# Performance work log

Measured on AMD Instinct MI355X. Metric: run time of the kernel, lower is better.

## Reference

```python
import jax, jax.numpy as jnp
import numpy as np

HIDDEN = 2048
FFN = 2048      # ffn_hidden_size (tp_size == 1)
E = 8           # moe_num_experts
TOP_K = 2       # moe_top_k
S = 2048        # number of tokens


def setup_inputs() -> dict:
    key = jax.random.key(0)
    k1, k2, k3, k4 = jax.random.split(key, 4)
    return {
        "hidden_states": jax.random.normal(k1, (S, HIDDEN), jnp.float32),
        "w_qkv": jax.random.normal(k2, (3 * E, HIDDEN), jnp.float32) * 0.02,
        "w1": jax.random.normal(k3, (E, HIDDEN, 2 * FFN), jnp.float32) * 0.02,
        "w2": jax.random.normal(k4, (E, FFN, HIDDEN), jnp.float32) * 0.02,
        "top_k": TOP_K,
    }


def reference(hidden_states, w_qkv, w1, w2, top_k):
    S, H = hidden_states.shape
    # --- ParallelAttention_router (gate), computed in fp32 as in the source ---
    mix = hidden_states @ w_qkv.T                                  # [S, 3E]
    q, k, v = jnp.split(mix.astype(jnp.float32), 3, axis=-1)       # each [S, E]
    # attn_weights[s,i,j] = q[s,i]*k[s,j]; softmax over j; logits = attn @ v
    attn = jax.nn.softmax(q[:, :, None] * k[:, None, :], axis=-1)  # [S, E, E]
    logits = jnp.einsum('sij,sj->si', attn, v)                     # [S, E]
    # --- top-k routing: softmax over selected logits ---
    top_logits, indices = jax.lax.top_k(logits, top_k)             # [S, K]
    scores = jax.nn.softmax(top_logits, axis=-1).astype(hidden_states.dtype)
    # --- experts: per-expert GLU MLP. The torch code sorts tokens by expert and
    # runs a grouped-GEMM loop; mathematically out[s] = sum_k scores[s,k] *
    # MLP_{indices[s,k]}(x[s]). We compute all experts densely (static shapes)
    # and gather/combine, which is the same math. ---
    fc1 = jnp.einsum('sh,ehi->esi', hidden_states, w1)             # [E, S, 2*FFN]
    g, u = jnp.split(fc1, 2, axis=-1)
    inter = jax.nn.silu(g) * u                                     # [E, S, FFN]
    expert_out = jnp.einsum('esi,eih->esh', inter, w2)             # [E, S, H]
    tok = jnp.arange(S)
    out = jnp.zeros_like(hidden_states)
    for kk in range(top_k):  # tiny static loop over top_k (=2)
        out = out + scores[:, kk, None] * expert_out[indices[:, kk], tok]
    return out
```

## Files before the change

kernel.cpp:

```cpp
#include <hip/hip_runtime.h>
#include <math.h>

#define S_TOK 2048
#define HID   2048
#define FFN_  2048
#define NEXP  8
#define NSLOT (S_TOK*2)

typedef short  s8v __attribute__((ext_vector_type(8)));
typedef short  s4v __attribute__((ext_vector_type(4)));
typedef float  f4v __attribute__((ext_vector_type(4)));

__device__ __forceinline__ unsigned short f32_bf16(float f){
  unsigned u = __float_as_uint(f);
  u += 0x7fffu + ((u>>16)&1u);
  return (unsigned short)(u>>16);
}
__device__ __forceinline__ int lds_off(int r,int kq){
  return (r*4 + (kq ^ ((r>>2)&3)))*8;
}

__global__ void init_k(int* hdr){
  if (threadIdx.x < 24) hdr[threadIdx.x] = 0;
}

__global__ __launch_bounds__(64) void router_k(
    const float* __restrict__ X, const float* __restrict__ Wqkv,
    int* __restrict__ hdr, int* __restrict__ idx, float* __restrict__ scr)
{
  const int s = blockIdx.x, lane = threadIdx.x;
  const float* x = X + (size_t)s*HID;
  f4v xv[8];
  #pragma unroll
  for (int i=0;i<8;i++) xv[i] = *reinterpret_cast<const f4v*>(x + (i*64+lane)*4);
  float dot[24];
  #pragma unroll
  for (int o=0;o<24;o++){
    const float* w = Wqkv + (size_t)o*HID;
    float a = 0.f;
    #pragma unroll
    for (int i=0;i<8;i++){
      f4v wv = *reinterpret_cast<const f4v*>(w + (i*64+lane)*4);
      a += xv[i][0]*wv[0] + xv[i][1]*wv[1] + xv[i][2]*wv[2] + xv[i][3]*wv[3];
    }
    #pragma unroll
    for (int off=32; off; off>>=1) a += __shfl_xor(a, off, 64);
    dot[o] = a;
  }
  if (lane==0){
    float lg[8];
    #pragma unroll
    for (int i=0;i<8;i++){
      float qi = dot[i];
      float mx = -1e30f;
      #pragma unroll
      for (int j=0;j<8;j++) mx = fmaxf(mx, qi*dot[8+j]);
      float se=0.f, lv=0.f;
      #pragma unroll
      for (int j=0;j<8;j++){
        float e = expf(qi*dot[8+j] - mx);
        se += e; lv += e*dot[16+j];
      }
      lg[i] = lv/se;
    }
    int i0=0; float v0=lg[0];
    #pragma unroll
    for (int i=1;i<8;i++) if (lg[i]>v0){v0=lg[i];i0=i;}
    int i1=-1; float v1=-1e30f;
    #pragma unroll
    for (int i=0;i<8;i++) if (i!=i0 && lg[i]>v1){v1=lg[i];i1=i;}
    float a  = expf(v1-v0);
    float s0 = 1.f/(1.f+a);
    idx[s*2]=i0; idx[s*2+1]=i1;
    scr[s*2]=s0; scr[s*2+1]=a*s0;
    atomicAdd(&hdr[i0],1); atomicAdd(&hdr[i1],1);
  }
}

__global__ void scan_k(int* hdr){
  if (threadIdx.x==0){
    int a=0;
    for (int e=0;e<NEXP;e++){ hdr[16+e]=a; a+=hdr[e]; }
  }
}

__global__ __launch_bounds__(256) void scatter_k(
    const int* __restrict__ idx, const float* __restrict__ scr, int* hdr,
    int* __restrict__ slot_of, int* __restrict__ tok_slot, float* __restrict__ scr_slot)
{
  int s = blockIdx.x*256 + threadIdx.x;
  if (s >= S_TOK) return;
  #pragma unroll
  for (int k=0;k<2;k++){
    int e    = idx[s*2+k];
    int pos  = atomicAdd(&hdr[8+e], 1);
    int slot = hdr[16+e] + pos;
    tok_slot[slot] = s;
    scr_slot[slot] = scr[s*2+k];
    slot_of[s*2+k] = slot;
  }
}

__global__ __launch_bounds__(256,2) void gemm1_k(
    const float* __restrict__ X, const float* __restrict__ W1,
    const int* __restrict__ hdr, const int* __restrict__ tok_slot,
    unsigned short* __restrict__ inter)
{
  const int e = blockIdx.z, mt = blockIdx.y, nt = blockIdx.x;
  const int cnt = hdr[e];
  const int m0  = mt*128;
  if (m0 >= cnt) return;
  const int off = hdr[16+e];
  const int n0  = nt*64;
  const float* W1e = W1 + (size_t)e*HID*(2*FFN_);

  __shared__ __align__(16) unsigned short sA[128*32];
  __shared__ __align__(16) unsigned short sB[128*32];
  __shared__ int sTok[128];

  const int tid = threadIdx.x;
  if (tid < 128){
    int r = m0 + tid; if (r >= cnt) r = cnt-1;
    sTok[tid] = tok_slot[off + r];
  }
  const int lane = tid & 63, wv = tid >> 6;
  const int wm = wv >> 1, wn = wv & 1;
  const int lm = lane & 15, kq = lane >> 4;
  const int b_cq = tid & 31, b_k4 = tid >> 5;
  const int b_j  = (b_cq<16) ? (n0 + b_cq*4) : (FFN_ + n0 + (b_cq-16)*4);
  const int b_n  = b_cq*4;

  f4v zero = {0.f,0.f,0.f,0.f};
  f4v acc[2][2][4];
  #pragma unroll
  for (int a=0;a<2;a++)
    #pragma unroll
    for (int b=0;b<2;b++)
      #pragma unroll
      for (int c=0;c<4;c++) acc[a][b][c]=zero;

  __syncthreads();

  for (int k0=0; k0<HID; k0+=32){
    #pragma unroll
    for (int i=0;i<4;i++){
      int v = tid + i*256;
      int m = v>>3, c4q = v&7;
      f4v f = *reinterpret_cast<const f4v*>(X + (size_t)sTok[m]*HID + k0 + c4q*4);
      s4v p; p[0]=(short)f32_bf16(f[0]); p[1]=(short)f32_bf16(f[1]);
             p[2]=(short)f32_bf16(f[2]); p[3]=(short)f32_bf16(f[3]);
      *reinterpret_cast<s4v*>(&sA[lds_off(m, c4q>>1) + (c4q&1)*4]) = p;
    }
    f4v bw[4];
    #pragma unroll
    for (int kk=0;kk<4;kk++)
      bw[kk] = *reinterpret_cast<const f4v*>(W1e + (size_t)(k0 + b_k4*4 + kk)*(2*FFN_) + b_j);
    #pragma unroll
    for (int jj=0;jj<4;jj++){
      int n = b_n + jj;
      s4v p; p[0]=(short)f32_bf16(bw[0][jj]); p[1]=(short)f32_bf16(bw[1][jj]);
             p[2]=(short)f32_bf16(bw[2][jj]); p[3]=(short)f32_bf16(bw[3][jj]);
      *reinterpret_cast<s4v*>(&sB[lds_off(n, b_k4>>1) + (b_k4&1)*4]) = p;
    }
    __syncthreads();
    s8v af[4], bf_[2][2];
    #pragma unroll
    for (int mf=0;mf<4;mf++)
      af[mf] = *reinterpret_cast<const s8v*>(&sA[lds_off(wm*64+mf*16+lm, kq)]);
    #pragma unroll
    for (int st=0; st<2; st++)
      #pragma unroll
      for (int nf=0;nf<2;nf++)
        bf_[st][nf] = *reinterpret_cast<const s8v*>(&sB[lds_off(st*64+wn*32+nf*16+lm, kq)]);
    #pragma unroll
    for (int st=0; st<2; st++)
      #pragma unroll
      for (int nf=0;nf<2;nf++)
        #pragma unroll
        for (int mf=0;mf<4;mf++)
          acc[st][nf][mf] = __builtin_amdgcn_mfma_f32_16x16x32_bf16(
              af[mf], bf_[st][nf], acc[st][nf][mf], 0,0,0);
    __syncthreads();
  }
  const int lq = lane>>4;
  #pragma unroll
  for (int nf=0;nf<2;nf++)
    #pragma unroll
    for (int mf=0;mf<4;mf++){
      f4v g = acc[0][nf][mf], u = acc[1][nf][mf];
      #pragma unroll
      for (int r=0;r<4;r++){
        int row = wm*64 + mf*16 + lq*4 + r;
        if (m0+row < cnt){
          float gv = g[r];
          float val = gv / (1.f + expf(-gv)) * u[r];
          inter[(size_t)(off+m0+row)*FFN_ + n0 + wn*32 + nf*16 + lm] = f32_bf16(val);
        }
      }
    }
}

__global__ __launch_bounds__(256,2) void gemm2_k(
    const unsigned short* __restrict__ inter, const float* __restrict__ W2,
    const int* __restrict__ hdr, const float* __restrict__ scr_slot,
    float* __restrict__ eout)
{
  const int e = blockIdx.z, mt = blockIdx.y, nt = blockIdx.x;
  const int cnt = hdr[e];
  const int m0  = mt*128;
  if (m0 >= cnt) return;
  const int off = hdr[16+e];
  const int n0  = nt*128;
  const float* W2e = W2 + (size_t)e*FFN_*HID;

  __shared__ __align__(16) unsigned short sA[128*32];
  __shared__ __align__(16) unsigned short sB[128*32];
  __shared__ float sScr[128];

  const int tid = threadIdx.x;
  if (tid < 128){
    int r = m0 + tid; if (r >= cnt) r = cnt-1;
    sScr[tid] = scr_slot[off + r];
  }
  const int lane = tid & 63, wv = tid >> 6;
  const int wm = wv >> 1, wn = wv & 1;
  const int lm = lane & 15, kq = lane >> 4;
  const int b_cq = tid & 31, b_k4 = tid >> 5;
  const int b_j  = n0 + b_cq*4;
  const int b_n  = b_cq*4;

  f4v zero = {0.f,0.f,0.f,0.f};
  f4v acc[4][4];
  #pragma unroll
  for (int a=0;a<4;a++)
    #pragma unroll
    for (int b=0;b<4;b++) acc[a][b]=zero;

  __syncthreads();

  for (int k0=0; k0<FFN_; k0+=32){
    #pragma unroll
    for (int i=0;i<2;i++){
      int v = tid + i*256;
      int m = v>>2, kk8 = v&3;
      int r = m0+m; if (r>=cnt) r = cnt-1;
      s8v a = *reinterpret_cast<const s8v*>(inter + (size_t)(off+r)*FFN_ + k0 + kk8*8);
      *reinterpret_cast<s8v*>(&sA[lds_off(m, kk8)]) = a;
    }
    f4v bw[4];
    #pragma unroll
    for (int kk=0;kk<4;kk++)
      bw[kk] = *reinterpret_cast<const f4v*>(W2e + (size_t)(k0 + b_k4*4 + kk)*HID + b_j);
    #pragma unroll
    for (int jj=0;jj<4;jj++){
      int n = b_n + jj;
      s4v p; p[0]=(short)f32_bf16(bw[0][jj]); p[1]=(short)f32_bf16(bw[1][jj]);
             p[2]=(short)f32_bf16(bw[2][jj]); p[3]=(short)f32_bf16(bw[3][jj]);
      *reinterpret_cast<s4v*>(&sB[lds_off(n, b_k4>>1) + (b_k4&1)*4]) = p;
    }
    __syncthreads();
    s8v af[4], bf_[4];
    #pragma unroll
    for (int mf=0;mf<4;mf++)
      af[mf] = *reinterpret_cast<const s8v*>(&sA[lds_off(wm*64+mf*16+lm, kq)]);
    #pragma unroll
    for (int nf=0;nf<4;nf++)
      bf_[nf] = *reinterpret_cast<const s8v*>(&sB[lds_off(wn*64+nf*16+lm, kq)]);
    #pragma unroll
    for (int nf=0;nf<4;nf++)
      #pragma unroll
      for (int mf=0;mf<4;mf++)
        acc[nf][mf] = __builtin_amdgcn_mfma_f32_16x16x32_bf16(
            af[mf], bf_[nf], acc[nf][mf], 0,0,0);
    __syncthreads();
  }
  const int lq = lane>>4;
  #pragma unroll
  for (int nf=0;nf<4;nf++)
    #pragma unroll
    for (int mf=0;mf<4;mf++)
      #pragma unroll
      for (int r=0;r<4;r++){
        int row = wm*64 + mf*16 + lq*4 + r;
        if (m0+row < cnt)
          eout[(size_t)(off+m0+row)*HID + n0 + wn*64 + nf*16 + lm] = acc[nf][mf][r]*sScr[row];
      }
}

__global__ __launch_bounds__(256) void combine_k(
    const float* __restrict__ eout, const int* __restrict__ slot_of,
    float* __restrict__ out)
{
  int s = blockIdx.x, tid = threadIdx.x;
  const float* a = eout + (size_t)slot_of[s*2]  *HID;
  const float* b = eout + (size_t)slot_of[s*2+1]*HID;
  float* o = out + (size_t)s*HID;
  #pragma unroll
  for (int v=tid; v<HID/4; v+=256){
    f4v x = *reinterpret_cast<const f4v*>(a + v*4);
    f4v y = *reinterpret_cast<const f4v*>(b + v*4);
    *reinterpret_cast<f4v*>(o + v*4) = x + y;
  }
}

extern "C" void kernel_launch(void* const* d_in, const int* in_sizes, int n_in,
                              void* d_out, int out_size, void* d_ws, size_t ws_size,
                              hipStream_t stream)
{
  const float* X    = (const float*)d_in[0];
  const float* Wqkv = (const float*)d_in[1];
  const float* W1   = (const float*)d_in[2];
  const float* W2   = (const float*)d_in[3];
  float* out = (float*)d_out;

  char* ws = (char*)d_ws;
  int*   hdr      = (int*)ws;
  int*   idx      = (int*)(ws + 256);
  float* scr      = (float*)(ws + 256 + 1*16384);
  int*   slot_of  = (int*)(ws + 256 + 2*16384);
  int*   tok_slot = (int*)(ws + 256 + 3*16384);
  float* scr_slot = (float*)(ws + 256 + 4*16384);
  unsigned short* inter = (unsigned short*)(ws + 82176);
  float* eout     = (float*)(ws + 82176 + (size_t)NSLOT*FFN_*2);

  init_k   <<<1,   64, 0, stream>>>(hdr);
  router_k <<<S_TOK,64,0, stream>>>(X, Wqkv, hdr, idx, scr);
  scan_k   <<<1,   64, 0, stream>>>(hdr);
  scatter_k<<<(S_TOK+255)/256, 256, 0, stream>>>(idx, scr, hdr, slot_of, tok_slot, scr_slot);
  gemm1_k  <<<dim3(FFN_/64,  S_TOK/128, NEXP), 256, 0, stream>>>(X, W1, hdr, tok_slot, inter);
  gemm2_k  <<<dim3(HID/128,  S_TOK/128, NEXP), 256, 0, stream>>>(inter, W2, hdr, scr_slot, eout);
  combine_k<<<S_TOK, 256, 0, stream>>>(eout, slot_of, out);
}
```

Baseline: 822.6 us.

## Pre-convert weights and activations to bf16 and stream tiles with global_load_lds

Adds a per-call transpose-and-convert kernel that writes W1 and W2 as K-contiguous bf16. The router now also writes a bf16 copy of X. Both grouped GEMMs then load tiles straight into LDS with global_load_lds, using a K=64 step and an XOR swizzle, and the grid is reordered so M tiles vary fastest. This removes per-tile fp32 loads and in-loop conversions and halves global traffic inside the GEMMs. In exchange it adds a full extra read and write pass over 384 MB of fp32 weights on every call.

```diff
diff --git a/kernel.cpp b/kernel.cpp
--- a/kernel.cpp
+++ b/kernel.cpp
@@ -16,8 +16,11 @@
   u += 0x7fffu + ((u>>16)&1u);
   return (unsigned short)(u>>16);
 }
-__device__ __forceinline__ int lds_off(int r,int kq){
-  return (r*4 + (kq ^ ((r>>2)&3)))*8;
+
+__device__ __forceinline__ void gload_lds16(const void* gp, void* lp){
+  __builtin_amdgcn_global_load_lds(
+      (const __attribute__((address_space(1))) unsigned int*)gp,
+      (__attribute__((address_space(3))) unsigned int*)lp, 16, 0, 0);
 }
 
 __global__ void init_k(int* hdr){
@@ -26,13 +29,20 @@
 
 __global__ __launch_bounds__(64) void router_k(
     const float* __restrict__ X, const float* __restrict__ Wqkv,
-    int* __restrict__ hdr, int* __restrict__ idx, float* __restrict__ scr)
+    int* __restrict__ hdr, int* __restrict__ idx, float* __restrict__ scr,
+    unsigned short* __restrict__ Xbf)
 {
   const int s = blockIdx.x, lane = threadIdx.x;
   const float* x = X + (size_t)s*HID;
   f4v xv[8];
   #pragma unroll
   for (int i=0;i<8;i++) xv[i] = *reinterpret_cast<const f4v*>(x + (i*64+lane)*4);
+  #pragma unroll
+  for (int i=0;i<8;i++){
+    s4v p; p[0]=(short)f32_bf16(xv[i][0]); p[1]=(short)f32_bf16(xv[i][1]);
+           p[2]=(short)f32_bf16(xv[i][2]); p[3]=(short)f32_bf16(xv[i][3]);
+    *reinterpret_cast<s4v*>(Xbf + (size_t)s*HID + (i*64+lane)*4) = p;
+  }
   float dot[24];
   #pragma unroll
   for (int o=0;o<24;o++){
@@ -101,21 +111,59 @@
   }
 }
 
+__global__ __launch_bounds__(256) void tconv_k(
+    const float* __restrict__ src, unsigned short* __restrict__ dst, int K, int N)
+{
+  const int e = blockIdx.z;
+  const int n0 = blockIdx.x*64, k0 = blockIdx.y*64;
+  const float* Sp = src + (size_t)e*K*N;
+  unsigned short* Dp = dst + (size_t)e*K*N;
+  __shared__ float sT[64*65];
+  const int t = threadIdx.x;
+  {
+    const int kr = t>>4, nc = (t&15)*4;
+    #pragma unroll
+    for (int i=0;i<4;i++){
+      int k = k0 + kr + i*16;
+      f4v v = *reinterpret_cast<const f4v*>(Sp + (size_t)k*N + n0 + nc);
+      sT[(nc+0)*65 + kr + i*16] = v[0];
+      sT[(nc+1)*65 + kr + i*16] = v[1];
+      sT[(nc+2)*65 + kr + i*16] = v[2];
+      sT[(nc+3)*65 + kr + i*16] = v[3];
+    }
+  }
+  __syncthreads();
+  {
+    const int nr = t>>4, kc = (t&15)*4;
+    #pragma unroll
+    for (int i=0;i<4;i++){
+      int n = nr + i*16;
+      s4v p;
+      p[0]=(short)f32_bf16(sT[n*65 + kc+0]);
+      p[1]=(short)f32_bf16(sT[n*65 + kc+1]);
+      p[2]=(short)f32_bf16(sT[n*65 + kc+2]);
+      p[3]=(short)f32_bf16(sT[n*65 + kc+3]);
+      *reinterpret_cast<s4v*>(Dp + (size_t)(n0+n)*K + k0 + kc) = p;
+    }
+  }
+}
+
+
 __global__ __launch_bounds__(256,2) void gemm1_k(
-    const float* __restrict__ X, const float* __restrict__ W1,
+    const unsigned short* __restrict__ Xbf, const unsigned short* __restrict__ W1t,
     const int* __restrict__ hdr, const int* __restrict__ tok_slot,
     unsigned short* __restrict__ inter)
 {
-  const int e = blockIdx.z, mt = blockIdx.y, nt = blockIdx.x;
+  const int e = blockIdx.z, mt = blockIdx.x, nt = blockIdx.y;
   const int cnt = hdr[e];
   const int m0  = mt*128;
   if (m0 >= cnt) return;
   const int off = hdr[16+e];
   const int n0  = nt*64;
-  const float* W1e = W1 + (size_t)e*HID*(2*FFN_);
-
-  __shared__ __align__(16) unsigned short sA[128*32];
-  __shared__ __align__(16) unsigned short sB[128*32];
+  const unsigned short* W1e = W1t + (size_t)e*HID*(2*FFN_);
+
+  __shared__ __align__(16) unsigned short sA[128*64];
+  __shared__ __align__(16) unsigned short sB[128*64];
   __shared__ int sTok[128];
 
   const int tid = threadIdx.x;
@@ -123,12 +171,21 @@
     int r = m0 + tid; if (r >= cnt) r = cnt-1;
     sTok[tid] = tok_slot[off + r];
   }
-  const int lane = tid & 63, wv = tid >> 6;
-  const int wm = wv >> 1, wn = wv & 1;
-  const int lm = lane & 15, kq = lane >> 4;
-  const int b_cq = tid & 31, b_k4 = tid >> 5;
-  const int b_j  = (b_cq<16) ? (n0 + b_cq*4) : (FFN_ + n0 + (b_cq-16)*4);
-  const int b_n  = b_cq*4;
+  __syncthreads();
+
+  const int lane = tid & 63, w = tid>>6;
+  const int wm = w>>1, wn = w&1;
+  const int lm = lane & 15, kq = lane>>4;
+
+  const unsigned short* gA[4]; const unsigned short* gB[4];
+  #pragma unroll
+  for (int i=0;i<4;i++){
+    int l = i*256 + tid;
+    int m = l>>3, cc = (l&7) ^ (m&7);
+    gA[i] = Xbf + (size_t)sTok[m]*HID + cc*8;
+    int col = (m<64) ? (n0+m) : (FFN_ + n0 + (m-64));
+    gB[i] = W1e + (size_t)col*HID + cc*8;
+  }
 
   f4v zero = {0.f,0.f,0.f,0.f};
   f4v acc[2][2][4];
@@ -139,47 +196,38 @@
       #pragma unroll
       for (int c=0;c<4;c++) acc[a][b][c]=zero;
 
-  __syncthreads();
-
-  for (int k0=0; k0<HID; k0+=32){
+  for (int k0=0; k0<HID; k0+=64){
     #pragma unroll
     for (int i=0;i<4;i++){
-      int v = tid + i*256;
-      int m = v>>3, c4q = v&7;
-      f4v f = *reinterpret_cast<const f4v*>(X + (size_t)sTok[m]*HID + k0 + c4q*4);
-      s4v p; p[0]=(short)f32_bf16(f[0]); p[1]=(short)f32_bf16(f[1]);
-             p[2]=(short)f32_bf16(f[2]); p[3]=(short)f32_bf16(f[3]);
-      *reinterpret_cast<s4v*>(&sA[lds_off(m, c4q>>1) + (c4q&1)*4]) = p;
-    }
-    f4v bw[4];
-    #pragma unroll
-    for (int kk=0;kk<4;kk++)
-      bw[kk] = *reinterpret_cast<const f4v*>(W1e + (size_t)(k0 + b_k4*4 + kk)*(2*FFN_) + b_j);
-    #pragma unroll
-    for (int jj=0;jj<4;jj++){
-      int n = b_n + jj;
-      s4v p; p[0]=(short)f32_bf16(bw[0][jj]); p[1]=(short)f32_bf16(bw[1][jj]);
-             p[2]=(short)f32_bf16(bw[2][jj]); p[3]=(short)f32_bf16(bw[3][jj]);
-      *reinterpret_cast<s4v*>(&sB[lds_off(n, b_k4>>1) + (b_k4&1)*4]) = p;
+      gload_lds16(gA[i] + k0, &sA[(i*256 + w*64)*8]);
+      gload_lds16(gB[i] + k0, &sB[(i*256 + w*64)*8]);
     }
     __syncthreads();
-    s8v af[4], bf_[2][2];
-    #pragma unroll
-    for (int mf=0;mf<4;mf++)
-      af[mf] = *reinterpret_cast<const s8v*>(&sA[lds_off(wm*64+mf*16+lm, kq)]);
-    #pragma unroll
-    for (int st=0; st<2; st++)
-      #pragma unroll
-      for (int nf=0;nf<2;nf++)
-        bf_[st][nf] = *reinterpret_cast<const s8v*>(&sB[lds_off(st*64+wn*32+nf*16+lm, kq)]);
-    #pragma unroll
-    for (int st=0; st<2; st++)
-      #pragma unroll
-      for (int nf=0;nf<2;nf++)
+    #pragma unroll
+    for (int ks=0; ks<2; ks++){
+      const int c = ks*4 + kq;
+      s8v af[4], bf_[2][2];
+      #pragma unroll
+      for (int mf=0;mf<4;mf++){
+        int m = wm*64 + mf*16 + lm;
+        af[mf] = *reinterpret_cast<const s8v*>(&sA[(m*8 + (c ^ (m&7)))*8]);
+      }
+      #pragma unroll
+      for (int st=0; st<2; st++)
         #pragma unroll
-        for (int mf=0;mf<4;mf++)
-          acc[st][nf][mf] = __builtin_amdgcn_mfma_f32_16x16x32_bf16(
-              af[mf], bf_[st][nf], acc[st][nf][mf], 0,0,0);
+        for (int nf=0;nf<2;nf++){
+          int n = st*64 + wn*32 + nf*16 + lm;
+          bf_[st][nf] = *reinterpret_cast<const s8v*>(&sB[(n*8 + (c ^ (n&7)))*8]);
+        }
+      #pragma unroll
+      for (int st=0; st<2; st++)
+        #pragma unroll
+        for (int nf=0;nf<2;nf++)
+          #pragma unroll
+          for (int mf=0;mf<4;mf++)
+            acc[st][nf][mf] = __builtin_amdgcn_mfma_f32_16x16x32_bf16(
+                af[mf], bf_[st][nf], acc[st][nf][mf], 0,0,0);
+    }
     __syncthreads();
   }
   const int lq = lane>>4;
@@ -201,20 +249,20 @@
 }
 
 __global__ __launch_bounds__(256,2) void gemm2_k(
-    const unsigned short* __restrict__ inter, const float* __restrict__ W2,
+    const unsigned short* __restrict__ inter, const unsigned short* __restrict__ W2t,
     const int* __restrict__ hdr, const float* __restrict__ scr_slot,
     float* __restrict__ eout)
 {
-  const int e = blockIdx.z, mt = blockIdx.y, nt = blockIdx.x;
+  const int e = blockIdx.z, mt = blockIdx.x, nt = blockIdx.y;
   const int cnt = hdr[e];
   const int m0  = mt*128;
   if (m0 >= cnt) return;
   const int off = hdr[16+e];
   const int n0  = nt*128;
-  const float* W2e = W2 + (size_t)e*FFN_*HID;
-
-  __shared__ __align__(16) unsigned short sA[128*32];
-  __shared__ __align__(16) unsigned short sB[128*32];
+  const unsigned short* W2e = W2t + (size_t)e*FFN_*HID;
+
+  __shared__ __align__(16) unsigned short sA[128*64];
+  __shared__ __align__(16) unsigned short sB[128*64];
   __shared__ float sScr[128];
 
   const int tid = threadIdx.x;
@@ -222,12 +270,21 @@
     int r = m0 + tid; if (r >= cnt) r = cnt-1;
     sScr[tid] = scr_slot[off + r];
   }
-  const int lane = tid & 63, wv = tid >> 6;
-  const int wm = wv >> 1, wn = wv & 1;
-  const int lm = lane & 15, kq = lane >> 4;
-  const int b_cq = tid & 31, b_k4 = tid >> 5;
-  const int b_j  = n0 + b_cq*4;
-  const int b_n  = b_cq*4;
+  __syncthreads();
+
+  const int lane = tid & 63, w = tid>>6;
+  const int wm = w>>1, wn = w&1;
+  const int lm = lane & 15, kq = lane>>4;
+
+  const unsigned short* gA[4]; const unsigned short* gB[4];
+  #pragma unroll
+  for (int i=0;i<4;i++){
+    int l = i*256 + tid;
+    int m = l>>3, cc = (l&7) ^ (m&7);
+    int r = m0 + m; if (r >= cnt) r = cnt-1;
+    gA[i] = inter + (size_t)(off+r)*FFN_ + cc*8;
+    gB[i] = W2e + (size_t)(n0+m)*FFN_ + cc*8;
+  }
 
   f4v zero = {0.f,0.f,0.f,0.f};
   f4v acc[4][4];
@@ -236,42 +293,34 @@
     #pragma unroll
     for (int b=0;b<4;b++) acc[a][b]=zero;
 
-  __syncthreads();
-
-  for (int k0=0; k0<FFN_; k0+=32){
-    #pragma unroll
-    for (int i=0;i<2;i++){
-      int v = tid + i*256;
-      int m = v>>2, kk8 = v&3;
-      int r = m0+m; if (r>=cnt) r = cnt-1;
-      s8v a = *reinterpret_cast<const s8v*>(inter + (size_t)(off+r)*FFN_ + k0 + kk8*8);
-      *reinterpret_cast<s8v*>(&sA[lds_off(m, kk8)]) = a;
-    }
-    f4v bw[4];
-    #pragma unroll
-    for (int kk=0;kk<4;kk++)
-      bw[kk] = *reinterpret_cast<const f4v*>(W2e + (size_t)(k0 + b_k4*4 + kk)*HID + b_j);
-    #pragma unroll
-    for (int jj=0;jj<4;jj++){
-      int n = b_n + jj;
-      s4v p; p[0]=(short)f32_bf16(bw[0][jj]); p[1]=(short)f32_bf16(bw[1][jj]);
-             p[2]=(short)f32_bf16(bw[2][jj]); p[3]=(short)f32_bf16(bw[3][jj]);
-      *reinterpret_cast<s4v*>(&sB[lds_off(n, b_k4>>1) + (b_k4&1)*4]) = p;
+  for (int k0=0; k0<FFN_; k0+=64){
+    #pragma unroll
+    for (int i=0;i<4;i++){
+      gload_lds16(gA[i] + k0, &sA[(i*256 + w*64)*8]);
+      gload_lds16(gB[i] + k0, &sB[(i*256 + w*64)*8]);
     }
     __syncthreads();
-    s8v af[4], bf_[4];
-    #pragma unroll
-    for (int mf=0;mf<4;mf++)
-      af[mf] = *reinterpret_cast<const s8v*>(&sA[lds_off(wm*64+mf*16+lm, kq)]);
-    #pragma unroll
-    for (int nf=0;nf<4;nf++)
-      bf_[nf] = *reinterpret_cast<const s8v*>(&sB[lds_off(wn*64+nf*16+lm, kq)]);
-    #pragma unroll
-    for (int nf=0;nf<4;nf++)
-      #pragma unroll
-      for (int mf=0;mf<4;mf++)
-        acc[nf][mf] = __builtin_amdgcn_mfma_f32_16x16x32_bf16(
-            af[mf], bf_[nf], acc[nf][mf], 0,0,0);
+    #pragma unroll
+    for (int ks=0; ks<2; ks++){
+      const int c = ks*4 + kq;
+      s8v af[4], bf_[4];
+      #pragma unroll
+      for (int mf=0;mf<4;mf++){
+        int m = wm*64 + mf*16 + lm;
+        af[mf] = *reinterpret_cast<const s8v*>(&sA[(m*8 + (c ^ (m&7)))*8]);
+      }
+      #pragma unroll
+      for (int nf=0;nf<4;nf++){
+        int n = wn*64 + nf*16 + lm;
+        bf_[nf] = *reinterpret_cast<const s8v*>(&sB[(n*8 + (c ^ (n&7)))*8]);
+      }
+      #pragma unroll
+      for (int nf=0;nf<4;nf++)
+        #pragma unroll
+        for (int mf=0;mf<4;mf++)
+          acc[nf][mf] = __builtin_amdgcn_mfma_f32_16x16x32_bf16(
+              af[mf], bf_[nf], acc[nf][mf], 0,0,0);
+    }
     __syncthreads();
   }
   const int lq = lane>>4;
@@ -314,20 +363,26 @@
   float* out = (float*)d_out;
 
   char* ws = (char*)d_ws;
-  int*   hdr      = (int*)ws;
-  int*   idx      = (int*)(ws + 256);
-  float* scr      = (float*)(ws + 256 + 1*16384);
-  int*   slot_of  = (int*)(ws + 256 + 2*16384);
-  int*   tok_slot = (int*)(ws + 256 + 3*16384);
-  float* scr_slot = (float*)(ws + 256 + 4*16384);
-  unsigned short* inter = (unsigned short*)(ws + 82176);
-  float* eout     = (float*)(ws + 82176 + (size_t)NSLOT*FFN_*2);
+  size_t o = 0;
+  int*   hdr      = (int*)(ws + o); o += 1024;
+  int*   idx      = (int*)(ws + o); o += (size_t)S_TOK*2*4;
+  float* scr      = (float*)(ws + o); o += (size_t)S_TOK*2*4;
+  int*   slot_of  = (int*)(ws + o); o += (size_t)S_TOK*2*4;
+  int*   tok_slot = (int*)(ws + o); o += (size_t)NSLOT*4;
+  float* scr_slot = (float*)(ws + o); o += (size_t)NSLOT*4;
+  unsigned short* Xbf  = (unsigned short*)(ws + o); o += (size_t)S_TOK*HID*2;
+  unsigned short* inter= (unsigned short*)(ws + o); o += (size_t)NSLOT*FFN_*2;
+  float* eout     = (float*)(ws + o); o += (size_t)NSLOT*HID*4;
+  unsigned short* W1t  = (unsigned short*)(ws + o); o += (size_t)NEXP*HID*2*FFN_*2;
+  unsigned short* W2t  = (unsigned short*)(ws + o); o += (size_t)NEXP*FFN_*HID*2;
 
   init_k   <<<1,   64, 0, stream>>>(hdr);
-  router_k <<<S_TOK,64,0, stream>>>(X, Wqkv, hdr, idx, scr);
+  router_k <<<S_TOK,64,0, stream>>>(X, Wqkv, hdr, idx, scr, Xbf);
   scan_k   <<<1,   64, 0, stream>>>(hdr);
   scatter_k<<<(S_TOK+255)/256, 256, 0, stream>>>(idx, scr, hdr, slot_of, tok_slot, scr_slot);
-  gemm1_k  <<<dim3(FFN_/64,  S_TOK/128, NEXP), 256, 0, stream>>>(X, W1, hdr, tok_slot, inter);
-  gemm2_k  <<<dim3(HID/128,  S_TOK/128, NEXP), 256, 0, stream>>>(inter, W2, hdr, scr_slot, eout);
+  tconv_k  <<<dim3(2*FFN_/64, HID/64, NEXP), 256, 0, stream>>>(W1, W1t, HID, 2*FFN_);
+  tconv_k  <<<dim3(HID/64,  FFN_/64, NEXP), 256, 0, stream>>>(W2, W2t, FFN_, HID);
+  gemm1_k  <<<dim3(S_TOK/128, FFN_/64, NEXP), 256, 0, stream>>>(Xbf, W1t, hdr, tok_slot, inter);
+  gemm2_k  <<<dim3(S_TOK/128, HID/128, NEXP), 256, 0, stream>>>(inter, W2t, hdr, scr_slot, eout);
   combine_k<<<S_TOK, 256, 0, stream>>>(eout, slot_of, out);
 }
```

Measured after the change: 987.9 us. 1.2x slower.
